# Optimization experiments

Measured on AMD Instinct MI355X. Metric: run time of the kernel, lower is better.

## Reference

```python
import jax, jax.numpy as jnp
import numpy as np

ALPHA = 0.1
NUM_CLASSES = 1000
B, D = 16384, 2048


def setup_inputs() -> dict:
    key = jax.random.key(0)
    k1, k2 = jax.random.split(key)
    x = jax.random.normal(k1, (B, D), dtype=jnp.float32)
    y = jax.random.randint(k2, (B,), 0, NUM_CLASSES)
    return {"x": x, "y": y}


def reference(x, y):
    # Per-class mean/std via a single segment reduction (equivalent to the
    # original masked loop over classes; torch .std(0) is unbiased, ddof=1).
    cnt = jax.ops.segment_sum(jnp.ones((x.shape[0],), x.dtype), y, num_segments=NUM_CLASSES)  # [C]
    s = jax.ops.segment_sum(x, y, num_segments=NUM_CLASSES)        # [C, D]
    sq = jax.ops.segment_sum(x * x, y, num_segments=NUM_CLASSES)   # [C, D]
    cnt_ = cnt[:, None]
    mean = s / cnt_
    var = (sq - cnt_ * mean * mean) / (cnt_ - 1.0)  # unbiased variance
    std = jnp.sqrt(jnp.maximum(var, 0.0))
    nk, pk = jax.random.split(jax.random.key(42))
    # torch.normal(mean, std).detach()
    class_noise = jax.lax.stop_gradient(mean + std * jax.random.normal(nk, mean.shape, x.dtype))
    index = jax.random.permutation(pk, x.shape[0])
    newY = y[index]
    out = (1.0 - ALPHA) * x + ALPHA * class_noise[newY]
    return out, newY
```

## Files before the change

kernel.cpp:

```cpp
#include <hip/hip_runtime.h>
#include <cstdint>
#include <cstddef>

#define B_ROWS 16384
#define D_COLS 2048
#define NCLS   1000
#define NBUCK  1024

__host__ __device__ __forceinline__ uint32_t rotl32(uint32_t v, int r) {
    return (v << r) | (v >> (32 - r));
}

__host__ __device__ inline void tf2x32(uint32_t k0, uint32_t k1,
                                       uint32_t x0, uint32_t x1,
                                       uint32_t& o0, uint32_t& o1) {
    uint32_t ks0 = k0, ks1 = k1, ks2 = k0 ^ k1 ^ 0x1BD11BDAu;
    x0 += ks0; x1 += ks1;
    x0 += x1; x1 = rotl32(x1, 13); x1 ^= x0;
    x0 += x1; x1 = rotl32(x1, 15); x1 ^= x0;
    x0 += x1; x1 = rotl32(x1, 26); x1 ^= x0;
    x0 += x1; x1 = rotl32(x1, 6);  x1 ^= x0;
    x0 += ks1; x1 += ks2 + 1u;
    x0 += x1; x1 = rotl32(x1, 17); x1 ^= x0;
    x0 += x1; x1 = rotl32(x1, 29); x1 ^= x0;
    x0 += x1; x1 = rotl32(x1, 16); x1 ^= x0;
    x0 += x1; x1 = rotl32(x1, 24); x1 ^= x0;
    x0 += ks2; x1 += ks0 + 2u;
    x0 += x1; x1 = rotl32(x1, 13); x1 ^= x0;
    x0 += x1; x1 = rotl32(x1, 15); x1 ^= x0;
    x0 += x1; x1 = rotl32(x1, 26); x1 ^= x0;
    x0 += x1; x1 = rotl32(x1, 6);  x1 ^= x0;
    x0 += ks0; x1 += ks1 + 3u;
    x0 += x1; x1 = rotl32(x1, 17); x1 ^= x0;
    x0 += x1; x1 = rotl32(x1, 29); x1 ^= x0;
    x0 += x1; x1 = rotl32(x1, 16); x1 ^= x0;
    x0 += x1; x1 = rotl32(x1, 24); x1 ^= x0;
    x0 += ks1; x1 += ks2 + 4u;
    x0 += x1; x1 = rotl32(x1, 13); x1 ^= x0;
    x0 += x1; x1 = rotl32(x1, 15); x1 ^= x0;
    x0 += x1; x1 = rotl32(x1, 26); x1 ^= x0;
    x0 += x1; x1 = rotl32(x1, 6);  x1 ^= x0;
    x0 += ks2; x1 += ks0 + 5u;
    o0 = x0; o1 = x1;
}

__device__ __forceinline__ float erfinv_f(float x) {
    float w = -log1pf(-x * x);
    float p;
    if (w < 5.0f) {
        w -= 2.5f;
        p = 2.81022636e-08f;
        p = fmaf(p, w, 3.43273939e-07f);
        p = fmaf(p, w, -3.5233877e-06f);
        p = fmaf(p, w, -4.39150654e-06f);
        p = fmaf(p, w, 0.00021858087f);
        p = fmaf(p, w, -0.00125372503f);
        p = fmaf(p, w, -0.00417768164f);
        p = fmaf(p, w, 0.246640727f);
        p = fmaf(p, w, 1.50140941f);
    } else {
        w = sqrtf(w) - 3.0f;
        p = -0.000200214257f;
        p = fmaf(p, w, 0.000100950558f);
        p = fmaf(p, w, 0.00134934322f);
        p = fmaf(p, w, -0.00367342844f);
        p = fmaf(p, w, 0.00573950773f);
        p = fmaf(p, w, -0.0076224613f);
        p = fmaf(p, w, 0.00943887047f);
        p = fmaf(p, w, 1.00167406f);
        p = fmaf(p, w, 2.83297682f);
    }
    return p * x;
}


__global__ void k_bits_hist(const int* __restrict__ y, int* __restrict__ cnt,
                            uint32_t* __restrict__ kAbits, uint32_t* __restrict__ kBbits,
                            int* __restrict__ bhA, int* __restrict__ bhB,
                            uint32_t s1_0, uint32_t s1_1,
                            uint32_t s2_0, uint32_t s2_1) {
    int i = blockIdx.x * 256 + threadIdx.x;
    atomicAdd(&cnt[y[i]], 1);
    uint32_t a, b;
    tf2x32(s1_0, s1_1, 0u, (uint32_t)i, a, b);
    uint32_t bitsA = a ^ b;
    kAbits[i] = bitsA;
    atomicAdd(&bhA[bitsA >> 22], 1);
    tf2x32(s2_0, s2_1, 0u, (uint32_t)i, a, b);
    uint32_t bitsB = a ^ b;
    kBbits[i] = bitsB;
    atomicAdd(&bhB[bitsB >> 22], 1);
}

__global__ void k_prefix3(const int* __restrict__ cnt, int* __restrict__ rowstart,
                          const int* __restrict__ bhA, int* __restrict__ bsA,
                          const int* __restrict__ bhB, int* __restrict__ bsB) {
    __shared__ int sm[1024];
    int t = threadIdx.x;
    const int* src; int* dst; int n;
    if (blockIdx.x == 0)      { src = cnt; dst = rowstart; n = NCLS; }
    else if (blockIdx.x == 1) { src = bhA; dst = bsA;      n = NBUCK; }
    else                      { src = bhB; dst = bsB;      n = NBUCK; }
    int v = (t < n) ? src[t] : 0;
    sm[t] = v;
    for (int off = 1; off < 1024; off <<= 1) {
        __syncthreads();
        int u = (t >= off) ? sm[t - off] : 0;
        __syncthreads();
        sm[t] += u;
    }
    if (t < n) dst[t] = sm[t] - v;
}

__global__ void k_scatter_all(const int* __restrict__ y,
                              const uint32_t* __restrict__ kAbits,
                              const uint32_t* __restrict__ kBbits,
                              const int* __restrict__ rowstart, int* __restrict__ rowpos,
                              int* __restrict__ rowlist,
                              const int* __restrict__ bsA, int* __restrict__ bposA,
                              int* __restrict__ memA,
                              const int* __restrict__ bsB, int* __restrict__ bposB,
                              int* __restrict__ memB) {
    int i = blockIdx.x * 256 + threadIdx.x;
    int c = y[i];
    int p = atomicAdd(&rowpos[c], 1);
    rowlist[rowstart[c] + p] = i;
    uint32_t bA = kAbits[i] >> 22;
    p = atomicAdd(&bposA[bA], 1);
    memA[bsA[bA] + p] = i;
    uint32_t bB = kBbits[i] >> 22;
    p = atomicAdd(&bposB[bB], 1);
    memB[bsB[bB] + p] = i;
}

__global__ void __launch_bounds__(256) k_class_sums(
        const float* __restrict__ x, const int* __restrict__ rowlist,
        const int* __restrict__ rowstart, const int* __restrict__ cnt,
        float* __restrict__ s, float* __restrict__ sq) {
    int c = blockIdx.x, h = blockIdx.y, t = threadIdx.x;
    int start = rowstart[c], n = cnt[c];
    const float4* xb = (const float4*)x + (size_t)h * 256 + t;
    float sx=0,sy=0,sz=0,sw=0, qx=0,qy=0,qz=0,qw=0;
    int r = 0;
    for (; r + 2 <= n; r += 2) {
        int row0 = rowlist[start + r];
        int row1 = rowlist[start + r + 1];
        float4 a = xb[(size_t)row0 * 512];
        float4 b = xb[(size_t)row1 * 512];
        sx += a.x; sy += a.y; sz += a.z; sw += a.w;
        qx = fmaf(a.x, a.x, qx); qy = fmaf(a.y, a.y, qy);
        qz = fmaf(a.z, a.z, qz); qw = fmaf(a.w, a.w, qw);
        sx += b.x; sy += b.y; sz += b.z; sw += b.w;
        qx = fmaf(b.x, b.x, qx); qy = fmaf(b.y, b.y, qy);
        qz = fmaf(b.z, b.z, qz); qw = fmaf(b.w, b.w, qw);
    }
    if (r < n) {
        int row = rowlist[start + r];
        float4 a = xb[(size_t)row * 512];
        sx += a.x; sy += a.y; sz += a.z; sw += a.w;
        qx = fmaf(a.x, a.x, qx); qy = fmaf(a.y, a.y, qy);
        qz = fmaf(a.z, a.z, qz); qw = fmaf(a.w, a.w, qw);
    }
    int o = c * 512 + h * 256 + t;
    ((float4*)s)[o]  = make_float4(sx, sy, sz, sw);
    ((float4*)sq)[o] = make_float4(qx, qy, qz, qw);
}

__global__ void k_noise(const float* __restrict__ s, const float* __restrict__ sq,
                        const int* __restrict__ cnt, float* __restrict__ noise,
                        uint32_t nk0, uint32_t nk1) {
    int n = blockIdx.x * 256 + threadIdx.x;
    uint32_t b1, b2;
    tf2x32(nk0, nk1, 0u, (uint32_t)n, b1, b2);
    uint32_t bits = b1 ^ b2;
    float f = __uint_as_float((bits >> 9) | 0x3f800000u) - 1.0f;
    const float LO = -0.99999994f;
    float u = fmaxf(LO, fmaf(f, 2.0f, LO));
    float nr = 1.41421356f * erfinv_f(u);
    int c = n >> 11;
    float cf = (float)cnt[c];
    float m = s[n] / cf;
    float var = (sq[n] - cf * m * m) / (cf - 1.0f);
    float sd = sqrtf(fmaxf(var, 0.0f));
    noise[n] = fmaf(sd, nr, m);
}

__global__ void k_rankAB(const uint32_t* __restrict__ kAbits,
                         const uint32_t* __restrict__ kBbits,
                         const int* __restrict__ bsA, const int* __restrict__ bhA,
                         const int* __restrict__ memA,
                         const int* __restrict__ bsB, const int* __restrict__ bhB,
                         const int* __restrict__ memB,
                         int* __restrict__ x1, int* __restrict__ rank2) {
    int i = blockIdx.x * 256 + threadIdx.x;
    uint32_t a = kAbits[i];
    {
        uint32_t b = a >> 22;
        int st = bsA[b], n = bhA[b];
        int ca = 0;
        for (int k = 0; k < n; k++) {
            int m = memA[st + k];
            uint32_t mb = kAbits[m];
            ca += (mb < a) || (mb == a && m < i);
        }
        x1[st + ca] = i;
    }
    uint32_t c = kBbits[i];
    {
        uint32_t b = c >> 22;
        int st = bsB[b], n = bhB[b];
        int cb = 0;
        for (int k = 0; k < n; k++) {
            int m = memB[st + k];
            uint32_t mb = kBbits[m];
            cb += (mb < c) || (mb == c && m < i);
        }
        rank2[i] = st + cb;
    }
}

__global__ void k_scatter2(const int* __restrict__ y, const int* __restrict__ x1,
                           const int* __restrict__ rank2, int* __restrict__ newY,
                           float* __restrict__ outTail) {
    int i = blockIdx.x * 256 + threadIdx.x;
    int v = y[x1[i]];
    int j = rank2[i];
    newY[j] = v;
    outTail[j] = (float)v;
}

__global__ void __launch_bounds__(256) k_final(
        const float* __restrict__ x, const float* __restrict__ noise,
        const int* __restrict__ newY, float* __restrict__ out) {
    int b = blockIdx.x, t = threadIdx.x;
    int ny = newY[b];
    const float4* xr = (const float4*)x + (size_t)b * (D_COLS / 4);
    const float4* nr = (const float4*)noise + (size_t)ny * (D_COLS / 4);
    float4* orow = (float4*)out + (size_t)b * (D_COLS / 4);
    float4 xa = xr[t], na = nr[t];
    float4 o;
    o.x = fmaf(0.1f, na.x, 0.9f * xa.x);
    o.y = fmaf(0.1f, na.y, 0.9f * xa.y);
    o.z = fmaf(0.1f, na.z, 0.9f * xa.z);
    o.w = fmaf(0.1f, na.w, 0.9f * xa.w);
    orow[t] = o;
    xa = xr[t + 256]; na = nr[t + 256];
    o.x = fmaf(0.1f, na.x, 0.9f * xa.x);
    o.y = fmaf(0.1f, na.y, 0.9f * xa.y);
    o.z = fmaf(0.1f, na.z, 0.9f * xa.z);
    o.w = fmaf(0.1f, na.w, 0.9f * xa.w);
    orow[t + 256] = o;
}

extern "C" void kernel_launch(void* const* d_in, const int* in_sizes, int n_in,
                              void* d_out, int out_size, void* d_ws, size_t ws_size,
                              hipStream_t stream) {
    const float* x = (const float*)d_in[0];
    const int* y = (const int*)d_in[1];
    float* out = (float*)d_out;
    float* outTail = out + (size_t)B_ROWS * D_COLS;

    char* ws = (char*)d_ws;
    float* s     = (float*)(ws);
    float* sq    = (float*)(ws + 8192000);
    float* noise = (float*)(ws + 16384000);
    int* ints = (int*)(ws + 24576000);
    int* cnt      = ints;
    int* rowpos   = ints + 1000;
    int* bhA      = ints + 2000;
    int* bposA    = ints + 3024;
    int* bhB      = ints + 4048;
    int* bposB    = ints + 5072;
    int* rowstart = ints + 6096;
    int* bsA      = ints + 7096;
    int* bsB      = ints + 8120;
    int* rowlist  = ints + 9144;
    int* memA     = ints + 25528;
    int* memB     = ints + 41912;
    int* x1       = ints + 58296;
    int* rank2    = ints + 74680;
    int* newY     = ints + 91064;
    uint32_t* kAbits = (uint32_t*)(ints + 107448);
    uint32_t* kBbits = (uint32_t*)(ints + 123832);

    hipMemsetAsync(cnt, 0, 6096 * sizeof(int), stream);

    uint32_t nk0, nk1, pk0, pk1, pn0, pn1, s1_0, s1_1, s2_0, s2_1;
    tf2x32(0u, 42u, 0u, 0u, nk0, nk1);
    tf2x32(0u, 42u, 0u, 1u, pk0, pk1);
    tf2x32(pk0, pk1, 0u, 0u, pn0, pn1);
    tf2x32(pk0, pk1, 0u, 1u, s1_0, s1_1);
    tf2x32(pn0, pn1, 0u, 1u, s2_0, s2_1);

    k_bits_hist<<<64, 256, 0, stream>>>(y, cnt, kAbits, kBbits, bhA, bhB,
                                        s1_0, s1_1, s2_0, s2_1);
    k_prefix3<<<3, 1024, 0, stream>>>(cnt, rowstart, bhA, bsA, bhB, bsB);
    k_scatter_all<<<64, 256, 0, stream>>>(y, kAbits, kBbits, rowstart, rowpos,
                                          rowlist, bsA, bposA, memA,
                                          bsB, bposB, memB);
    k_class_sums<<<dim3(NCLS, 2), 256, 0, stream>>>(x, rowlist, rowstart, cnt, s, sq);
    k_noise<<<8000, 256, 0, stream>>>(s, sq, cnt, noise, nk0, nk1);
    k_rankAB<<<64, 256, 0, stream>>>(kAbits, kBbits, bsA, bhA, memA,
                                     bsB, bhB, memB, x1, rank2);
    k_scatter2<<<64, 256, 0, stream>>>(y, x1, rank2, newY, outTail);
    k_final<<<16384, 256, 0, stream>>>(x, noise, newY, out);
}
```

Before: 323.5 us.

## Fuse class sums, noise generation and rank kernels; use nontemporal output stores

Merges the per-class sum kernel and the noise kernel so the mean/std and random normal noise are computed in registers and written once. The s and sq intermediates no longer round-trip through memory. The rank computation runs as extra blocks in the same launch so it overlaps with the class reduction, removing two launches. The final output writes use nontemporal stores to avoid polluting cache with streaming output, though the noise index mapping must still match the original element order.

```diff
diff --git a/kernel.cpp b/kernel.cpp
--- a/kernel.cpp
+++ b/kernel.cpp
@@ -6,6 +6,13 @@
 #define D_COLS 2048
 #define NCLS   1000
 #define NBUCK  1024
+
+typedef float f4v __attribute__((ext_vector_type(4)));
+
+__device__ __forceinline__ void nt_store_f4(float4* p, float4 v) {
+    __builtin_nontemporal_store(*reinterpret_cast<f4v*>(&v),
+                                reinterpret_cast<f4v*>(p));
+}
 
 __host__ __device__ __forceinline__ uint32_t rotl32(uint32_t v, int r) {
     return (v << r) | (v >> (32 - r));
@@ -133,89 +140,90 @@
     memB[bsB[bB] + p] = i;
 }
 
-__global__ void __launch_bounds__(256) k_class_sums(
+__global__ void __launch_bounds__(256) k_mid(
         const float* __restrict__ x, const int* __restrict__ rowlist,
         const int* __restrict__ rowstart, const int* __restrict__ cnt,
-        float* __restrict__ s, float* __restrict__ sq) {
-    int c = blockIdx.x, h = blockIdx.y, t = threadIdx.x;
-    int start = rowstart[c], n = cnt[c];
-    const float4* xb = (const float4*)x + (size_t)h * 256 + t;
-    float sx=0,sy=0,sz=0,sw=0, qx=0,qy=0,qz=0,qw=0;
-    int r = 0;
-    for (; r + 2 <= n; r += 2) {
-        int row0 = rowlist[start + r];
-        int row1 = rowlist[start + r + 1];
-        float4 a = xb[(size_t)row0 * 512];
-        float4 b = xb[(size_t)row1 * 512];
-        sx += a.x; sy += a.y; sz += a.z; sw += a.w;
-        qx = fmaf(a.x, a.x, qx); qy = fmaf(a.y, a.y, qy);
-        qz = fmaf(a.z, a.z, qz); qw = fmaf(a.w, a.w, qw);
-        sx += b.x; sy += b.y; sz += b.z; sw += b.w;
-        qx = fmaf(b.x, b.x, qx); qy = fmaf(b.y, b.y, qy);
-        qz = fmaf(b.z, b.z, qz); qw = fmaf(b.w, b.w, qw);
-    }
-    if (r < n) {
-        int row = rowlist[start + r];
-        float4 a = xb[(size_t)row * 512];
-        sx += a.x; sy += a.y; sz += a.z; sw += a.w;
-        qx = fmaf(a.x, a.x, qx); qy = fmaf(a.y, a.y, qy);
-        qz = fmaf(a.z, a.z, qz); qw = fmaf(a.w, a.w, qw);
-    }
-    int o = c * 512 + h * 256 + t;
-    ((float4*)s)[o]  = make_float4(sx, sy, sz, sw);
-    ((float4*)sq)[o] = make_float4(qx, qy, qz, qw);
-}
-
-__global__ void k_noise(const float* __restrict__ s, const float* __restrict__ sq,
-                        const int* __restrict__ cnt, float* __restrict__ noise,
-                        uint32_t nk0, uint32_t nk1) {
-    int n = blockIdx.x * 256 + threadIdx.x;
-    uint32_t b1, b2;
-    tf2x32(nk0, nk1, 0u, (uint32_t)n, b1, b2);
-    uint32_t bits = b1 ^ b2;
-    float f = __uint_as_float((bits >> 9) | 0x3f800000u) - 1.0f;
-    const float LO = -0.99999994f;
-    float u = fmaxf(LO, fmaf(f, 2.0f, LO));
-    float nr = 1.41421356f * erfinv_f(u);
-    int c = n >> 11;
-    float cf = (float)cnt[c];
-    float m = s[n] / cf;
-    float var = (sq[n] - cf * m * m) / (cf - 1.0f);
-    float sd = sqrtf(fmaxf(var, 0.0f));
-    noise[n] = fmaf(sd, nr, m);
-}
-
-__global__ void k_rankAB(const uint32_t* __restrict__ kAbits,
-                         const uint32_t* __restrict__ kBbits,
-                         const int* __restrict__ bsA, const int* __restrict__ bhA,
-                         const int* __restrict__ memA,
-                         const int* __restrict__ bsB, const int* __restrict__ bhB,
-                         const int* __restrict__ memB,
-                         int* __restrict__ x1, int* __restrict__ rank2) {
-    int i = blockIdx.x * 256 + threadIdx.x;
-    uint32_t a = kAbits[i];
-    {
-        uint32_t b = a >> 22;
-        int st = bsA[b], n = bhA[b];
-        int ca = 0;
-        for (int k = 0; k < n; k++) {
-            int m = memA[st + k];
-            uint32_t mb = kAbits[m];
-            ca += (mb < a) || (mb == a && m < i);
-        }
-        x1[st + ca] = i;
-    }
-    uint32_t c = kBbits[i];
-    {
-        uint32_t b = c >> 22;
-        int st = bsB[b], n = bhB[b];
-        int cb = 0;
-        for (int k = 0; k < n; k++) {
-            int m = memB[st + k];
-            uint32_t mb = kBbits[m];
-            cb += (mb < c) || (mb == c && m < i);
-        }
-        rank2[i] = st + cb;
+        float* __restrict__ noise, uint32_t nk0, uint32_t nk1,
+        const uint32_t* __restrict__ kAbits, const uint32_t* __restrict__ kBbits,
+        const int* __restrict__ bsA, const int* __restrict__ bhA,
+        const int* __restrict__ memA,
+        const int* __restrict__ bsB, const int* __restrict__ bhB,
+        const int* __restrict__ memB,
+        int* __restrict__ x1, int* __restrict__ rank2) {
+    int bid = blockIdx.x, t = threadIdx.x;
+    if (bid >= 64) {
+        int cb = bid - 64;
+        int c = cb >> 1, h = cb & 1;
+        int start = rowstart[c], n = cnt[c];
+        const float4* xb = (const float4*)x + (size_t)h * 256 + t;
+        float sx=0,sy=0,sz=0,sw=0, qx=0,qy=0,qz=0,qw=0;
+        int r = 0;
+        for (; r + 2 <= n; r += 2) {
+            int row0 = rowlist[start + r];
+            int row1 = rowlist[start + r + 1];
+            float4 a = xb[(size_t)row0 * 512];
+            float4 b = xb[(size_t)row1 * 512];
+            sx += a.x; sy += a.y; sz += a.z; sw += a.w;
+            qx = fmaf(a.x, a.x, qx); qy = fmaf(a.y, a.y, qy);
+            qz = fmaf(a.z, a.z, qz); qw = fmaf(a.w, a.w, qw);
+            sx += b.x; sy += b.y; sz += b.z; sw += b.w;
+            qx = fmaf(b.x, b.x, qx); qy = fmaf(b.y, b.y, qy);
+            qz = fmaf(b.z, b.z, qz); qw = fmaf(b.w, b.w, qw);
+        }
+        if (r < n) {
+            int row = rowlist[start + r];
+            float4 a = xb[(size_t)row * 512];
+            sx += a.x; sy += a.y; sz += a.z; sw += a.w;
+            qx = fmaf(a.x, a.x, qx); qy = fmaf(a.y, a.y, qy);
+            qz = fmaf(a.z, a.z, qz); qw = fmaf(a.w, a.w, qw);
+        }
+        float sarr[4] = {sx, sy, sz, sw};
+        float qarr[4] = {qx, qy, qz, qw};
+        float oarr[4];
+        float cf = (float)n;
+        uint32_t nbase = (uint32_t)(c * 2048 + h * 1024 + t * 4);
+        #pragma unroll
+        for (int j = 0; j < 4; ++j) {
+            uint32_t b1, b2;
+            tf2x32(nk0, nk1, 0u, nbase + (uint32_t)j, b1, b2);
+            uint32_t bits = b1 ^ b2;
+            float f = __uint_as_float((bits >> 9) | 0x3f800000u) - 1.0f;
+            const float LO = -0.99999994f;
+            float u = fmaxf(LO, fmaf(f, 2.0f, LO));
+            float nrm = 1.41421356f * erfinv_f(u);
+            float m = sarr[j] / cf;
+            float var = (qarr[j] - cf * m * m) / (cf - 1.0f);
+            float sd = sqrtf(fmaxf(var, 0.0f));
+            oarr[j] = fmaf(sd, nrm, m);
+        }
+        int o = c * 512 + h * 256 + t;
+        ((float4*)noise)[o] = make_float4(oarr[0], oarr[1], oarr[2], oarr[3]);
+    } else {
+        int i = bid * 256 + t;
+        uint32_t a = kAbits[i];
+        {
+            uint32_t b = a >> 22;
+            int st = bsA[b], n = bhA[b];
+            int ca = 0;
+            for (int k = 0; k < n; k++) {
+                int m = memA[st + k];
+                uint32_t mb = kAbits[m];
+                ca += (mb < a) || (mb == a && m < i);
+            }
+            x1[st + ca] = i;
+        }
+        uint32_t c = kBbits[i];
+        {
+            uint32_t b = c >> 22;
+            int st = bsB[b], n = bhB[b];
+            int cb = 0;
+            for (int k = 0; k < n; k++) {
+                int m = memB[st + k];
+                uint32_t mb = kBbits[m];
+                cb += (mb < c) || (mb == c && m < i);
+            }
+            rank2[i] = st + cb;
+        }
     }
 }
 
@@ -243,13 +251,13 @@
     o.y = fmaf(0.1f, na.y, 0.9f * xa.y);
     o.z = fmaf(0.1f, na.z, 0.9f * xa.z);
     o.w = fmaf(0.1f, na.w, 0.9f * xa.w);
-    orow[t] = o;
+    nt_store_f4(&orow[t], o);
     xa = xr[t + 256]; na = nr[t + 256];
     o.x = fmaf(0.1f, na.x, 0.9f * xa.x);
     o.y = fmaf(0.1f, na.y, 0.9f * xa.y);
     o.z = fmaf(0.1f, na.z, 0.9f * xa.z);
     o.w = fmaf(0.1f, na.w, 0.9f * xa.w);
-    orow[t + 256] = o;
+    nt_store_f4(&orow[t + 256], o);
 }
 
 extern "C" void kernel_launch(void* const* d_in, const int* in_sizes, int n_in,
@@ -261,8 +269,6 @@
     float* outTail = out + (size_t)B_ROWS * D_COLS;
 
     char* ws = (char*)d_ws;
-    float* s     = (float*)(ws);
-    float* sq    = (float*)(ws + 8192000);
     float* noise = (float*)(ws + 16384000);
     int* ints = (int*)(ws + 24576000);
     int* cnt      = ints;
@@ -298,10 +304,11 @@
     k_scatter_all<<<64, 256, 0, stream>>>(y, kAbits, kBbits, rowstart, rowpos,
                                           rowlist, bsA, bposA, memA,
                                           bsB, bposB, memB);
-    k_class_sums<<<dim3(NCLS, 2), 256, 0, stream>>>(x, rowlist, rowstart, cnt, s, sq);
-    k_noise<<<8000, 256, 0, stream>>>(s, sq, cnt, noise, nk0, nk1);
-    k_rankAB<<<64, 256, 0, stream>>>(kAbits, kBbits, bsA, bhA, memA,
-                                     bsB, bhB, memB, x1, rank2);
+    k_mid<<<2 * NCLS + 64, 256, 0, stream>>>(x, rowlist, rowstart, cnt,
+                                             noise, nk0, nk1,
+                                             kAbits, kBbits,
+                                             bsA, bhA, memA,
+                                             bsB, bhB, memB, x1, rank2);
     k_scatter2<<<64, 256, 0, stream>>>(y, x1, rank2, newY, outTail);
     k_final<<<16384, 256, 0, stream>>>(x, noise, newY, out);
 }
```

After: 299.5 us, median of 2. 7.4% less time.
